# Kernel tuning notes

Hardware: AMD Instinct MI355X
Metric: run time of the kernel (lower is better)

Reference implementation:

```python
import jax, jax.numpy as jnp
import numpy as np

B, S, D_MODEL = 1, 2048, 2048
H, KVH = 16, 4
HD = D_MODEL // H          # 128
N_REP = H // KVH           # 4 (GQA)
WINDOW = 1024              # window_size=(WINDOW-1, 0): self + 1023 past tokens
CLIP = 8.0
THETA = 500000.0
EPS = 1e-6
SCALE = 1.0 / (HD ** 0.5)


def rms_norm(x, w):
    # per-head RMSNorm over last dim (head_dim)
    var = jnp.mean(jnp.square(x), axis=-1, keepdims=True)
    return x * jax.lax.rsqrt(var + EPS) * w


def rope_tables():
    inv_freq = 1.0 / (THETA ** (jnp.arange(0, HD, 2, dtype=jnp.float32) / HD))
    pos = jnp.arange(S, dtype=jnp.float32)
    freqs = pos[:, None] * inv_freq[None, :]          # [S, HD/2]
    emb = jnp.concatenate([freqs, freqs], axis=-1)    # [S, HD]
    return jnp.cos(emb), jnp.sin(emb)


def rotate_half(x):
    x1, x2 = x[..., : HD // 2], x[..., HD // 2 :]
    return jnp.concatenate([-x2, x1], axis=-1)


def apply_rope(x, cos, sin):
    # x: [B, S, h, HD]; cos/sin: [S, HD]
    return x * cos[None, :, None, :] + rotate_half(x) * sin[None, :, None, :]


def setup_inputs() -> dict:
    key = jax.random.key(0)
    ks = jax.random.split(key, 7)
    w = lambda k, shape: jax.random.normal(k, shape, jnp.float32) * 0.02
    return {
        "x": jax.random.normal(ks[0], (B, S, D_MODEL), jnp.float32),
        "w_q": w(ks[1], (D_MODEL, D_MODEL)),
        "w_k": w(ks[2], (KVH * HD, D_MODEL)),
        "w_v": w(ks[3], (KVH * HD, D_MODEL)),
        "w_out": w(ks[4], (D_MODEL, D_MODEL)),
        "q_norm_w": jnp.ones((HD,), jnp.float32),
        "k_norm_w": jnp.ones((HD,), jnp.float32),
        "sinks": jax.random.normal(ks[5], (H,), jnp.float32),
    }


def reference(x, w_q, w_k, w_v, w_out, q_norm_w, k_norm_w, sinks):
    # fused QKV projection + clip
    q = jnp.clip(x @ w_q.T, -CLIP, CLIP).reshape(B, S, H, HD)
    k = jnp.clip(x @ w_k.T, -CLIP, CLIP).reshape(B, S, KVH, HD)
    v = jnp.clip(x @ w_v.T, -CLIP, CLIP).reshape(B, S, KVH, HD)

    # per-head qk RMSNorm, then RoPE
    q = rms_norm(q, q_norm_w)
    k = rms_norm(k, k_norm_w)
    cos, sin = rope_tables()
    q = apply_rope(q, cos, sin)
    k = apply_rope(k, cos, sin)

    # GQA: repeat_interleave kv heads
    k = jnp.repeat(k, N_REP, axis=2)  # [B, S, H, HD]
    v = jnp.repeat(v, N_REP, axis=2)

    # sliding-window causal attention with a learned per-head sink logit
    logits = jnp.einsum("bqhd,bkhd->bhqk", q, k) * SCALE  # [B, H, S, S]
    qi = jnp.arange(S)[:, None]
    ki = jnp.arange(S)[None, :]
    mask = (ki <= qi) & (ki > qi - WINDOW)                # causal + window
    logits = jnp.where(mask[None, None, :, :], logits, -jnp.inf)

    # sink token: always-visible extra logit sinks[h] with zero value vector
    sink_col = jnp.broadcast_to(sinks[None, :, None, None], (B, H, S, 1))
    full = jnp.concatenate([logits, sink_col], axis=-1)   # [B, H, S, S+1]
    probs = jax.nn.softmax(full, axis=-1)

    att = jnp.einsum("bhqk,bkhd->bqhd", probs[..., :S], v)  # sink value is 0
    return att.reshape(B, S, D_MODEL) @ w_out.T
```

## Files before the change

kernel.cpp:

```cpp
#include <hip/hip_runtime.h>
#include <hip/hip_bf16.h>
#include <math.h>

#define S_LEN 2048
#define DMODEL 2048
#define NH 16
#define NKVH 4
#define HDIM 128
#define WINDOW 1024

typedef __bf16 bf16;
typedef __bf16 bf16x8 __attribute__((ext_vector_type(8)));
typedef __bf16 bf16x4 __attribute__((ext_vector_type(4)));
typedef float floatx4 __attribute__((ext_vector_type(4)));

static __device__ __forceinline__ bf16x8 load_bf8(const bf16* p) {
    return *reinterpret_cast<const bf16x8*>(p);
}

static __device__ __forceinline__ void async16(const bf16* g, bf16* l) {
    __builtin_amdgcn_global_load_lds(
        (const __attribute__((address_space(1))) void*)g,
        (__attribute__((address_space(3))) void*)l, 16, 0, 0);
}

__global__ __launch_bounds__(256) void convert_kernel(
    const float* __restrict__ x, const float* __restrict__ wq,
    const float* __restrict__ wk, const float* __restrict__ wv,
    const float* __restrict__ wo,
    bf16* __restrict__ xb, bf16* __restrict__ wqb, bf16* __restrict__ wkb,
    bf16* __restrict__ wvb, bf16* __restrict__ wob) {
    int i = blockIdx.x * blockDim.x + threadIdx.x;
    const float* src; bf16* dst; int off;
    if      (i < 1048576) { src = x;  dst = xb;  off = i; }
    else if (i < 2097152) { src = wq; dst = wqb; off = i - 1048576; }
    else if (i < 2359296) { src = wk; dst = wkb; off = i - 2097152; }
    else if (i < 2621440) { src = wv; dst = wvb; off = i - 2359296; }
    else if (i < 3670016) { src = wo; dst = wob; off = i - 2621440; }
    else return;
    float4 v = reinterpret_cast<const float4*>(src)[off];
    union { bf16 b[4]; ushort4 u; } t;
    t.b[0] = (bf16)v.x; t.b[1] = (bf16)v.y; t.b[2] = (bf16)v.z; t.b[3] = (bf16)v.w;
    reinterpret_cast<ushort4*>(dst)[off] = t.u;
}

#define GEMM_BODY(EXTRA_LDS_DECLS)                                             \
    __shared__ __align__(16) bf16 smem[4 * 128 * 64];               \
    EXTRA_LDS_DECLS                                                            \
    int tid = threadIdx.x;                                                     \
    int lane = tid & 63, wid = tid >> 6;                                       \
    int l15 = lane & 15, quad = lane >> 4;                                     \
    int rlocal = lane >> 3;                                                    \
    int scol = ((lane & 7) ^ rlocal) * 8;                                      \
    const bf16* gA = A + (size_t)(m0 + wid * 32 + rlocal) * K + scol;          \
    const bf16* gB = B + (size_t)(n0 + wid * 32 + rlocal) * K + scol;          \
    int ldsOf = (wid * 32) * 64;                                               \
    floatx4 acc[4][4];                                                         \
    _Pragma("unroll") for (int mi = 0; mi < 4; ++mi)                           \
        _Pragma("unroll") for (int ni = 0; ni < 4; ++ni)                       \
            acc[mi][ni] = floatx4{0.f, 0.f, 0.f, 0.f};                         \
    int mb = (wid & 1) * 64, nb = (wid >> 1) * 64;                             \
    _Pragma("unroll") for (int j = 0; j < 4; ++j) {                            \
        async16(gA + (size_t)(j * 8) * K, smem + ldsOf + j * 512);             \
        async16(gB + (size_t)(j * 8) * K, smem + 16384 + ldsOf + j * 512);     \
    }                                                                          \
    int buf = 0;                                                               \
    for (int k0 = 0; k0 < K; k0 += 64) {                                       \
        __syncthreads();                                                       \
        if (k0 + 64 < K) {                                                     \
            int nof = (buf ^ 1) * 8192;                                        \
            _Pragma("unroll") for (int j = 0; j < 4; ++j) {                    \
                async16(gA + (size_t)(j * 8) * K + k0 + 64,                    \
                        smem + nof + ldsOf + j * 512);                         \
                async16(gB + (size_t)(j * 8) * K + k0 + 64,                    \
                        smem + 16384 + nof + ldsOf + j * 512);                 \
            }                                                                  \
        }                                                                      \
        const bf16* sA = smem + buf * 8192;                                    \
        const bf16* sB = smem + 16384 + buf * 8192;                            \
        _Pragma("unroll") for (int kc = 0; kc < 2; ++kc) {                     \
            bf16x8 af[4], bq[4];                                               \
            _Pragma("unroll") for (int i = 0; i < 4; ++i) {                    \
                int ch = ((kc << 2) + quad) ^ (l15 & 7);                       \
                af[i] = load_bf8(sA + (mb + i * 16 + l15) * 64 + ch * 8);      \
                bq[i] = load_bf8(sB + (nb + i * 16 + l15) * 64 + ch * 8);      \
            }                                                                  \
            _Pragma("unroll") for (int mi = 0; mi < 4; ++mi)                   \
                _Pragma("unroll") for (int ni = 0; ni < 4; ++ni)               \
                    acc[mi][ni] = __builtin_amdgcn_mfma_f32_16x16x32_bf16(     \
                        af[mi], bq[ni], acc[mi][ni], 0, 0, 0);                 \
        }                                                                      \
        buf ^= 1;                                                              \
    }

__global__ __launch_bounds__(256) void gemm_qkv_fused(
    const bf16* __restrict__ A, const bf16* __restrict__ B,
    const float* __restrict__ qw, const float* __restrict__ kw,
    bf16* __restrict__ qb, bf16* __restrict__ kb, bf16* __restrict__ vtb) {
    const int K = 2048;
    int m0 = blockIdx.y * 128, n0 = blockIdx.x * 128;
    GEMM_BODY(__shared__ float rowss[128][2];)

#pragma unroll
    for (int mi = 0; mi < 4; ++mi)
#pragma unroll
        for (int ni = 0; ni < 4; ++ni)
#pragma unroll
            for (int r = 0; r < 4; ++r)
                acc[mi][ni][r] = fminf(fmaxf(acc[mi][ni][r], -8.0f), 8.0f);

    if (n0 >= 2560) {
#pragma unroll
        for (int mi = 0; mi < 4; ++mi)
#pragma unroll
            for (int ni = 0; ni < 4; ++ni)
#pragma unroll
                for (int r = 0; r < 4; ++r) {
                    int row = m0 + mb + mi * 16 + quad * 4 + r;
                    int n = n0 + nb + ni * 16 + l15;
                    vtb[(size_t)(n - 2560) * 2048 + row] = (bf16)acc[mi][ni][r];
                }
        return;
    }

    __syncthreads();
    bf16 (*xnorm)[128] = (bf16(*)[128])(smem + 16384);

#pragma unroll
    for (int mi = 0; mi < 4; ++mi)
#pragma unroll
        for (int r = 0; r < 4; ++r) {
            float s = 0.f;
#pragma unroll
            for (int ni = 0; ni < 4; ++ni) s += acc[mi][ni][r] * acc[mi][ni][r];
#pragma unroll
            for (int o = 1; o < 16; o <<= 1) s += __shfl_xor(s, o, 64);
            if (l15 == 0) rowss[mb + mi * 16 + quad * 4 + r][wid >> 1] = s;
        }
    __syncthreads();

    const float* nw = (n0 < 2048) ? qw : kw;
#pragma unroll
    for (int mi = 0; mi < 4; ++mi)
#pragma unroll
        for (int r = 0; r < 4; ++r) {
            int row = mb + mi * 16 + quad * 4 + r;
            float var = (rowss[row][0] + rowss[row][1]) * (1.0f / 128.0f);
            float rinv = rsqrtf(var + 1e-6f);
#pragma unroll
            for (int ni = 0; ni < 4; ++ni) {
                int col = nb + ni * 16 + l15;
                float xn = acc[mi][ni][r] * rinv * nw[col];
                acc[mi][ni][r] = xn;
                xnorm[row][col] = (bf16)xn;
            }
        }
    __syncthreads();

    float invf[4];
#pragma unroll
    for (int ni = 0; ni < 4; ++ni) {
        int fi = (nb + ni * 16 + l15) & 63;
        invf[ni] = __expf((float)fi * (-13.122363377404328f / 64.0f));
    }
    bool lowhalf = (nb == 0);
#pragma unroll
    for (int mi = 0; mi < 4; ++mi)
#pragma unroll
        for (int r = 0; r < 4; ++r) {
            int row = mb + mi * 16 + quad * 4 + r;
            float pos = (float)(m0 + row);
#pragma unroll
            for (int ni = 0; ni < 4; ++ni) {
                int col = nb + ni * 16 + l15;
                float ang = pos * invf[ni];
                float c = __cosf(ang), sn = __sinf(ang);
                float part = (float)xnorm[row][col ^ 64];
                float rot = lowhalf ? -part : part;
                float o = acc[mi][ni][r] * c + rot * sn;
                int n = n0 + col;
                int s = m0 + row;
                if (n0 < 2048) qb[(size_t)s * 2048 + n] = (bf16)o;
                else           kb[(size_t)s * 512 + (n - 2048)] = (bf16)o;
            }
        }
}

__global__ __launch_bounds__(256) void gemm_out(
    const bf16* __restrict__ A, const bf16* __restrict__ B,
    float* __restrict__ C) {
    const int K = 2048, N = 2048;
    int m0 = blockIdx.y * 128, n0 = blockIdx.x * 128;
    GEMM_BODY()
#pragma unroll
    for (int mi = 0; mi < 4; ++mi)
#pragma unroll
        for (int ni = 0; ni < 4; ++ni)
#pragma unroll
            for (int r = 0; r < 4; ++r) {
                int m = m0 + mb + mi * 16 + quad * 4 + r;
                int n = n0 + nb + ni * 16 + l15;
                C[(size_t)m * N + n] = acc[mi][ni][r];
            }
}

__global__ __launch_bounds__(256) void attn(
    const bf16* __restrict__ qb, const bf16* __restrict__ kb,
    const bf16* __restrict__ vtb, const float* __restrict__ sinks,
    bf16* __restrict__ attb) {
    __shared__ __align__(16) bf16 sK[2][64 * 128];
    __shared__ __align__(16) bf16 sV[2][128 * 64];
    __shared__ __align__(16) bf16 sP[64 * 72];
    __shared__ float redu[64][4];
    int tid = threadIdx.x;
    int lane = tid & 63, wid = tid >> 6;
    int l15 = lane & 15, quad = lane >> 4;
    int h = blockIdx.y, kh = h >> 2;
    int bq0 = blockIdx.x * 64;

    bf16x8 qf[4][4];
#pragma unroll
    for (int ni = 0; ni < 4; ++ni) {
        const bf16* qrow = qb + (size_t)(bq0 + ni * 16 + l15) * 2048 + h * 128 + quad * 8;
#pragma unroll
        for (int kc = 0; kc < 4; ++kc) qf[ni][kc] = load_bf8(qrow + kc * 32);
    }

    floatx4 acc[4][2];
#pragma unroll
    for (int mi = 0; mi < 4; ++mi)
#pragma unroll
        for (int df = 0; df < 2; ++df) acc[mi][df] = floatx4{0.f, 0.f, 0.f, 0.f};
    float lpq[4];
#pragma unroll
    for (int ni = 0; ni < 4; ++ni) lpq[ni] = 0.f;

    int keyit = wid * 4 + (lane >> 4);
    int gcK = (lane & 15) ^ keyit;
    int dimit = wid * 8 + (lane >> 3);
    int gcV = (lane & 7) ^ ((lane >> 3) & 7);

    int tstart = bq0 - 1024; if (tstart < 0) tstart = 0;
    const bf16* kbase = kb + (size_t)kh * 128;
    const bf16* vbase = vtb + (size_t)kh * 128 * 2048;

#pragma unroll
    for (int r = 0; r < 4; ++r) {
        async16(kbase + (size_t)(tstart + r * 16 + keyit) * 512 + gcK * 8,
                sK[0] + (r * 16 + wid * 4) * 128);
        async16(vbase + (size_t)(r * 32 + dimit) * 2048 + tstart + gcV * 8,
                sV[0] + (r * 32 + wid * 8) * 64);
    }

    int buf = 0;
    for (int t = tstart; t <= bq0; t += 64) {
        __syncthreads();
        if (t + 64 <= bq0) {
#pragma unroll
            for (int r = 0; r < 4; ++r) {
                async16(kbase + (size_t)(t + 64 + r * 16 + keyit) * 512 + gcK * 8,
                        sK[buf ^ 1] + (r * 16 + wid * 4) * 128);
                async16(vbase + (size_t)(r * 32 + dimit) * 2048 + t + 64 + gcV * 8,
                        sV[buf ^ 1] + (r * 32 + wid * 8) * 64);
            }
        }
        floatx4 ST[4];
#pragma unroll
        for (int ni = 0; ni < 4; ++ni) ST[ni] = floatx4{0.f, 0.f, 0.f, 0.f};
#pragma unroll
        for (int kc = 0; kc < 4; ++kc) {
            int ch = (kc * 4 + quad) ^ l15;
            bf16x8 kf = load_bf8(sK[buf] + (wid * 16 + l15) * 128 + ch * 8);
#pragma unroll
            for (int ni = 0; ni < 4; ++ni)
                ST[ni] = __builtin_amdgcn_mfma_f32_16x16x32_bf16(kf, qf[ni][kc], ST[ni], 0, 0, 0);
        }
        int kbi = t + wid * 16 + quad * 4;
#pragma unroll
        for (int ni = 0; ni < 4; ++ni) {
            int qi = bq0 + ni * 16 + l15;
            bf16x4 pv;
#pragma unroll
            for (int r = 0; r < 4; ++r) {
                int ki = kbi + r;
                float v = ST[ni][r] * 0.08838834764831845f;
                bool ok = (ki <= qi) && (ki > qi - WINDOW);
                float e = ok ? __expf(v) : 0.0f;
                lpq[ni] += e;
                pv[r] = (bf16)e;
            }
            *(bf16x4*)(sP + (ni * 16 + l15) * 72 + wid * 16 + quad * 4) = pv;
        }
        __syncthreads();
#pragma unroll
        for (int kc = 0; kc < 2; ++kc) {
            bf16x8 pf[4];
#pragma unroll
            for (int mi = 0; mi < 4; ++mi)
                pf[mi] = load_bf8(sP + (mi * 16 + l15) * 72 + kc * 32 + quad * 8);
#pragma unroll
            for (int df = 0; df < 2; ++df) {
                int dim = wid * 32 + df * 16 + l15;
                int ch = (kc * 4 + quad) ^ (l15 & 7);
                bf16x8 vf = load_bf8(sV[buf] + dim * 64 + ch * 8);
#pragma unroll
                for (int mi = 0; mi < 4; ++mi)
                    acc[mi][df] = __builtin_amdgcn_mfma_f32_16x16x32_bf16(pf[mi], vf, acc[mi][df], 0, 0, 0);
            }
        }
        buf ^= 1;
    }

#pragma unroll
    for (int ni = 0; ni < 4; ++ni) {
        float v = lpq[ni];
        v += __shfl_xor(v, 16, 64);
        v += __shfl_xor(v, 32, 64);
        if (quad == 0) redu[ni * 16 + l15][wid] = v;
    }
    __syncthreads();
    float sk = __expf(sinks[h]);
#pragma unroll
    for (int mi = 0; mi < 4; ++mi)
#pragma unroll
        for (int r = 0; r < 4; ++r) {
            int row = mi * 16 + quad * 4 + r;
            float rs = redu[row][0] + redu[row][1] + redu[row][2] + redu[row][3] + sk;
            float inv = 1.0f / rs;
#pragma unroll
            for (int df = 0; df < 2; ++df) {
                int dim = wid * 32 + df * 16 + l15;
                attb[(size_t)(bq0 + row) * 2048 + h * 128 + dim] =
                    (bf16)(acc[mi][df][r] * inv);
            }
        }
}

extern "C" void kernel_launch(void* const* d_in, const int* in_sizes, int n_in,
                              void* d_out, int out_size, void* d_ws, size_t ws_size,
                              hipStream_t stream) {
    const float* x      = (const float*)d_in[0];
    const float* w_q    = (const float*)d_in[1];
    const float* w_k    = (const float*)d_in[2];
    const float* w_v    = (const float*)d_in[3];
    const float* w_out  = (const float*)d_in[4];
    const float* q_norm = (const float*)d_in[5];
    const float* k_norm = (const float*)d_in[6];
    const float* sinks  = (const float*)d_in[7];

    char* ws = (char*)d_ws;
    const size_t MB = 1u << 20;
    bf16* xb   = (bf16*)(ws + 0 * MB);
    bf16* wqb  = (bf16*)(ws + 8 * MB);
    bf16* wkb  = (bf16*)(ws + 16 * MB);
    bf16* wvb  = (bf16*)(ws + 18 * MB);
    bf16* wob  = (bf16*)(ws + 20 * MB);
    bf16* qb   = (bf16*)(ws + 28 * MB);
    bf16* kb   = (bf16*)(ws + 36 * MB);
    bf16* vtb  = (bf16*)(ws + 38 * MB);
    bf16* attb = (bf16*)(ws + 40 * MB);
    bf16* wcomb = wqb;
    float* out = (float*)d_out;

    convert_kernel<<<14336, 256, 0, stream>>>(x, w_q, w_k, w_v, w_out,
                                              xb, wqb, wkb, wvb, wob);
    gemm_qkv_fused<<<dim3(24, 16), 256, 0, stream>>>(xb, wcomb, q_norm, k_norm,
                                                     qb, kb, vtb);
    attn<<<dim3(32, 16), 256, 0, stream>>>(qb, kb, vtb, sinks, attb);
    gemm_out<<<dim3(16, 16), 256, 0, stream>>>(attb, wob, out);
}
```

Measured before the change: 208.7 us.

## Use 8-wave 128x256 GEMM tiles with triple-buffered async LDS pipeline

Rewrites the shared GEMM body so each block has 8 waves computing a 128x256 tile, with a 3-stage global-to-LDS async prefetch ring, explicit vmcnt waits, barriers interleaved with the MFMA phases, and setprio around the MFMA bursts. The QKV-fused and output GEMMs get half as many blocks, each twice as wide, and the norm/RoPE epilogue is adjusted so two heads share one tile. The aim is to hide load latency and raise MFMA utilisation. The cost is fewer blocks (192 and 128) on a large-CU GPU, which may leave CUs idle, plus higher LDS use and more barriers.

```diff
diff --git a/kernel.cpp b/kernel.cpp
--- a/kernel.cpp
+++ b/kernel.cpp
@@ -44,62 +44,77 @@
     reinterpret_cast<ushort4*>(dst)[off] = t.u;
 }
 
-#define GEMM_BODY(EXTRA_LDS_DECLS)                                             \
-    __shared__ __align__(16) bf16 smem[4 * 128 * 64];               \
-    EXTRA_LDS_DECLS                                                            \
+#define GEMM8_BODY()                                                           \
+    __shared__ __align__(16) bf16 smem[3 * 24576];  \
     int tid = threadIdx.x;                                                     \
     int lane = tid & 63, wid = tid >> 6;                                       \
     int l15 = lane & 15, quad = lane >> 4;                                     \
     int rlocal = lane >> 3;                                                    \
     int scol = ((lane & 7) ^ rlocal) * 8;                                      \
-    const bf16* gA = A + (size_t)(m0 + wid * 32 + rlocal) * K + scol;          \
-    const bf16* gB = B + (size_t)(n0 + wid * 32 + rlocal) * K + scol;          \
-    int ldsOf = (wid * 32) * 64;                                               \
+    const bf16* gA = A + (size_t)(m0 + wid * 16 + rlocal) * 2048 + scol;       \
+    const bf16* gB = B + (size_t)(n0 + wid * 32 + rlocal) * 2048 + scol;       \
+    int mb = (wid & 1) * 64, nb = (wid >> 1) * 64;                             \
     floatx4 acc[4][4];                                                         \
     _Pragma("unroll") for (int mi = 0; mi < 4; ++mi)                           \
         _Pragma("unroll") for (int ni = 0; ni < 4; ++ni)                       \
             acc[mi][ni] = floatx4{0.f, 0.f, 0.f, 0.f};                         \
-    int mb = (wid & 1) * 64, nb = (wid >> 1) * 64;                             \
-    _Pragma("unroll") for (int j = 0; j < 4; ++j) {                            \
-        async16(gA + (size_t)(j * 8) * K, smem + ldsOf + j * 512);             \
-        async16(gB + (size_t)(j * 8) * K, smem + 16384 + ldsOf + j * 512);     \
+             \
+    _Pragma("unroll") for (int s = 0; s < 2; ++s) {                            \
+        bf16* dA = smem + s * 24576 + wid * 1024;                              \
+        bf16* dB = smem + s * 24576 + 8192 + wid * 2048;                       \
+        _Pragma("unroll") for (int j = 0; j < 2; ++j)                          \
+            async16(gA + (size_t)(j * 8) * 2048 + s * 64, dA + j * 512);       \
+        _Pragma("unroll") for (int j = 0; j < 4; ++j)                          \
+            async16(gB + (size_t)(j * 8) * 2048 + s * 64, dB + j * 512);       \
     }                                                                          \
-    int buf = 0;                                                               \
-    for (int k0 = 0; k0 < K; k0 += 64) {                                       \
-        __syncthreads();                                                       \
-        if (k0 + 64 < K) {                                                     \
-            int nof = (buf ^ 1) * 8192;                                        \
-            _Pragma("unroll") for (int j = 0; j < 4; ++j) {                    \
-                async16(gA + (size_t)(j * 8) * K + k0 + 64,                    \
-                        smem + nof + ldsOf + j * 512);                         \
-                async16(gB + (size_t)(j * 8) * K + k0 + 64,                    \
-                        smem + 16384 + nof + ldsOf + j * 512);                 \
+    asm volatile("s_waitcnt vmcnt(6)" ::: "memory");         \
+    __builtin_amdgcn_s_barrier();                                              \
+    int slot = 0;                                                              \
+    _Pragma("unroll 1") for (int t = 0; t < 32; ++t) {                         \
+        if (t < 30) {   \
+            int s2 = slot + 2; if (s2 >= 3) s2 -= 3;                           \
+            bf16* dA = smem + s2 * 24576 + wid * 1024;                         \
+            bf16* dB = smem + s2 * 24576 + 8192 + wid * 2048;                  \
+            int kof = (t + 2) * 64;                                            \
+            _Pragma("unroll") for (int j = 0; j < 2; ++j)                      \
+                async16(gA + (size_t)(j * 8) * 2048 + kof, dA + j * 512);      \
+            _Pragma("unroll") for (int j = 0; j < 4; ++j)                      \
+                async16(gB + (size_t)(j * 8) * 2048 + kof, dB + j * 512);      \
+        }                                                                      \
+        const bf16* sA = smem + slot * 24576;                                  \
+        const bf16* sB = sA + 8192;                                            \
+        _Pragma("unroll") for (int kc = 0; kc < 2; ++kc)                       \
+            _Pragma("unroll") for (int mh = 0; mh < 2; ++mh) {                 \
+                int ch = ((kc << 2) + quad) ^ (l15 & 7);                       \
+                bf16x8 af[2], bq[4];                                           \
+                _Pragma("unroll") for (int i = 0; i < 2; ++i)                  \
+                    af[i] = load_bf8(sA + (mb + (mh * 2 + i) * 16 + l15) * 64  \
+                                     + ch * 8);                                \
+                _Pragma("unroll") for (int n = 0; n < 4; ++n)                  \
+                    bq[n] = load_bf8(sB + (nb + n * 16 + l15) * 64 + ch * 8);  \
+                __builtin_amdgcn_s_barrier();                                  \
+                __builtin_amdgcn_s_setprio(1);                                 \
+                _Pragma("unroll") for (int i = 0; i < 2; ++i)                  \
+                    _Pragma("unroll") for (int n = 0; n < 4; ++n)              \
+                        acc[mh * 2 + i][n] =                                   \
+                            __builtin_amdgcn_mfma_f32_16x16x32_bf16(           \
+                                af[i], bq[n], acc[mh * 2 + i][n], 0, 0, 0);    \
+                __builtin_amdgcn_s_setprio(0);                                 \
+                __builtin_amdgcn_s_barrier();                                  \
             }                                                                  \
-        }                                                                      \
-        const bf16* sA = smem + buf * 8192;                                    \
-        const bf16* sB = smem + 16384 + buf * 8192;                            \
-        _Pragma("unroll") for (int kc = 0; kc < 2; ++kc) {                     \
-            bf16x8 af[4], bq[4];                                               \
-            _Pragma("unroll") for (int i = 0; i < 4; ++i) {                    \
-                int ch = ((kc << 2) + quad) ^ (l15 & 7);                       \
-                af[i] = load_bf8(sA + (mb + i * 16 + l15) * 64 + ch * 8);      \
-                bq[i] = load_bf8(sB + (nb + i * 16 + l15) * 64 + ch * 8);      \
-            }                                                                  \
-            _Pragma("unroll") for (int mi = 0; mi < 4; ++mi)                   \
-                _Pragma("unroll") for (int ni = 0; ni < 4; ++ni)               \
-                    acc[mi][ni] = __builtin_amdgcn_mfma_f32_16x16x32_bf16(     \
-                        af[mi], bq[ni], acc[mi][ni], 0, 0, 0);                 \
-        }                                                                      \
-        buf ^= 1;                                                              \
-    }
-
-__global__ __launch_bounds__(256) void gemm_qkv_fused(
+        if (t < 30) { asm volatile("s_waitcnt vmcnt(6)" ::: "memory"); }       \
+        else        { asm volatile("s_waitcnt vmcnt(0)" ::: "memory"); }       \
+        __builtin_amdgcn_s_barrier();                                          \
+        __builtin_amdgcn_sched_barrier(0);                                     \
+        ++slot; if (slot == 3) slot = 0;                                       \
+    }
+
+__global__ __launch_bounds__(512) void gemm_qkv_fused(
     const bf16* __restrict__ A, const bf16* __restrict__ B,
     const float* __restrict__ qw, const float* __restrict__ kw,
     bf16* __restrict__ qb, bf16* __restrict__ kb, bf16* __restrict__ vtb) {
-    const int K = 2048;
-    int m0 = blockIdx.y * 128, n0 = blockIdx.x * 128;
-    GEMM_BODY(__shared__ float rowss[128][2];)
+    int m0 = blockIdx.y * 128, n0 = blockIdx.x * 256;
+    GEMM8_BODY()
 
 #pragma unroll
     for (int mi = 0; mi < 4; ++mi)
@@ -124,7 +139,8 @@
     }
 
     __syncthreads();
-    bf16 (*xnorm)[128] = (bf16(*)[128])(smem + 16384);
+    bf16 (*xnorm)[256] = (bf16(*)[256])smem;
+    float (*rowss)[4] = (float(*)[4])(smem + 32768);
 
 #pragma unroll
     for (int mi = 0; mi < 4; ++mi)
@@ -140,17 +156,19 @@
     __syncthreads();
 
     const float* nw = (n0 < 2048) ? qw : kw;
+    int hs = (wid >> 1) >> 1;
 #pragma unroll
     for (int mi = 0; mi < 4; ++mi)
 #pragma unroll
         for (int r = 0; r < 4; ++r) {
             int row = mb + mi * 16 + quad * 4 + r;
-            float var = (rowss[row][0] + rowss[row][1]) * (1.0f / 128.0f);
+            float var = (rowss[row][hs * 2] + rowss[row][hs * 2 + 1]) *
+                        (1.0f / 128.0f);
             float rinv = rsqrtf(var + 1e-6f);
 #pragma unroll
             for (int ni = 0; ni < 4; ++ni) {
                 int col = nb + ni * 16 + l15;
-                float xn = acc[mi][ni][r] * rinv * nw[col];
+                float xn = acc[mi][ni][r] * rinv * nw[col & 127];
                 acc[mi][ni][r] = xn;
                 xnorm[row][col] = (bf16)xn;
             }
@@ -163,7 +181,7 @@
         int fi = (nb + ni * 16 + l15) & 63;
         invf[ni] = __expf((float)fi * (-13.122363377404328f / 64.0f));
     }
-    bool lowhalf = (nb == 0);
+    bool lowhalf = ((nb & 127) == 0);
 #pragma unroll
     for (int mi = 0; mi < 4; ++mi)
 #pragma unroll
@@ -186,12 +204,12 @@
         }
 }
 
-__global__ __launch_bounds__(256) void gemm_out(
+__global__ __launch_bounds__(512) void gemm_out(
     const bf16* __restrict__ A, const bf16* __restrict__ B,
     float* __restrict__ C) {
-    const int K = 2048, N = 2048;
-    int m0 = blockIdx.y * 128, n0 = blockIdx.x * 128;
-    GEMM_BODY()
+    const int N = 2048;
+    int m0 = blockIdx.y * 128, n0 = blockIdx.x * 256;
+    GEMM8_BODY()
 #pragma unroll
     for (int mi = 0; mi < 4; ++mi)
 #pragma unroll
@@ -364,8 +382,8 @@
 
     convert_kernel<<<14336, 256, 0, stream>>>(x, w_q, w_k, w_v, w_out,
                                               xb, wqb, wkb, wvb, wob);
-    gemm_qkv_fused<<<dim3(24, 16), 256, 0, stream>>>(xb, wcomb, q_norm, k_norm,
+    gemm_qkv_fused<<<dim3(12, 16), 512, 0, stream>>>(xb, wcomb, q_norm, k_norm,
                                                      qb, kb, vtb);
     attn<<<dim3(32, 16), 256, 0, stream>>>(qb, kb, vtb, sinks, attb);
-    gemm_out<<<dim3(16, 16), 256, 0, stream>>>(attb, wob, out);
-}
+    gemm_out<<<dim3(8, 16), 512, 0, stream>>>(attb, wob, out);
+}
```

Measured after the change: 230.7 us. +10.5%, slower.
